# Kernel tuning notes

Measured on AMD Instinct MI355X. Metric: run time of the kernel, lower is better.

The kernel has to match this reference:

```python
import jax, jax.numpy as jnp
import numpy as np

N_EMBD = 1024
N_HEAD = 16
HEAD_DIM = N_EMBD // N_HEAD
D_FF = 4 * N_EMBD
B, T = 2, 2048


def setup_inputs() -> dict:
    key = jax.random.key(0)
    ks = jax.random.split(key, 16)
    s = 0.02
    d = {
        'x': jax.random.normal(ks[0], (B, T, N_EMBD), jnp.float32),
        'ln1_g': jnp.ones((N_EMBD,), jnp.float32),
        'ln1_b': jnp.zeros((N_EMBD,), jnp.float32),
        'Wq': jax.random.normal(ks[1], (N_EMBD, N_EMBD), jnp.float32) * s,
        'bq': jnp.zeros((N_EMBD,), jnp.float32),
        'Wk': jax.random.normal(ks[2], (N_EMBD, N_EMBD), jnp.float32) * s,
        'bk': jnp.zeros((N_EMBD,), jnp.float32),
        'Wv': jax.random.normal(ks[3], (N_EMBD, N_EMBD), jnp.float32) * s,
        'bv': jnp.zeros((N_EMBD,), jnp.float32),
        'Wo': jax.random.normal(ks[4], (N_EMBD, N_EMBD), jnp.float32) * s,
        'bo': jnp.zeros((N_EMBD,), jnp.float32),
        'ln2_g': jnp.ones((N_EMBD,), jnp.float32),
        'ln2_b': jnp.zeros((N_EMBD,), jnp.float32),
        'W1': jax.random.normal(ks[5], (N_EMBD, D_FF), jnp.float32) * s,
        'b1': jnp.zeros((D_FF,), jnp.float32),
        'W2': jax.random.normal(ks[6], (D_FF, N_EMBD), jnp.float32) * s,
        'b2': jnp.zeros((N_EMBD,), jnp.float32),
    }
    return d


def _layernorm(x, g, b, eps=1e-5):
    mu = jnp.mean(x, axis=-1, keepdims=True)
    var = jnp.var(x, axis=-1, keepdims=True)
    return (x - mu) * jax.lax.rsqrt(var + eps) * g + b


def _attention(x, Wq, bq, Wk, bk, Wv, bv, Wo, bo):
    b, t, c = x.shape
    q = (x @ Wq + bq).reshape(b, t, N_HEAD, HEAD_DIM).transpose(0, 2, 1, 3)
    k = (x @ Wk + bk).reshape(b, t, N_HEAD, HEAD_DIM).transpose(0, 2, 1, 3)
    v = (x @ Wv + bv).reshape(b, t, N_HEAD, HEAD_DIM).transpose(0, 2, 1, 3)
    att = jnp.einsum('bhqd,bhkd->bhqk', q, k) / jnp.sqrt(jnp.float32(HEAD_DIM))
    causal = jnp.tril(jnp.ones((t, t), bool))
    att = jnp.where(causal[None, None], att, -jnp.inf)
    att = jax.nn.softmax(att, axis=-1)
    y = jnp.einsum('bhqk,bhkd->bhqd', att, v)
    y = y.transpose(0, 2, 1, 3).reshape(b, t, c)
    return y @ Wo + bo


def reference(x, ln1_g, ln1_b, Wq, bq, Wk, bk, Wv, bv, Wo, bo, ln2_g, ln2_b, W1, b1, W2, b2):
    x = x + _attention(_layernorm(x, ln1_g, ln1_b), Wq, bq, Wk, bk, Wv, bv, Wo, bo)
    h = _layernorm(x, ln2_g, ln2_b)
    h = jax.nn.gelu(h @ W1 + b1, approximate=False) @ W2 + b2
    return x + h
```

## Files before the change

### kernel.cpp

```cpp
#include <hip/hip_runtime.h>
#include <hip/hip_bf16.h>

typedef __hip_bfloat16 bf16;
using bf16x8 = __attribute__((ext_vector_type(8))) short;
using f32x4  = __attribute__((ext_vector_type(4))) float;
using f32x16 = __attribute__((ext_vector_type(16))) float;
using u32x4  = __attribute__((ext_vector_type(4))) unsigned int;

#define TSEQ 2048
#define NH   16
#define HD   64
#define NC   1024
#define DFF  4096
#define NROWS 4096

__device__ __forceinline__ void load_lds16(const bf16* g, bf16* l) {
  __builtin_amdgcn_global_load_lds(
      (const __attribute__((address_space(1))) unsigned int*)g,
      (__attribute__((address_space(3))) unsigned int*)l, 16, 0, 0);
}

__device__ __forceinline__ float b2f(short s) {
  unsigned int u = ((unsigned int)(unsigned short)s) << 16;
  return __builtin_bit_cast(float, u);
}

__device__ __forceinline__ unsigned cvtpk(float a, float b) {
  unsigned r;
  asm("v_cvt_pk_bf16_f32 %0, %1, %2" : "=v"(r) : "v"(a), "v"(b));
  return r;
}

__device__ __forceinline__ void pl32swap(unsigned &d, unsigned &s) {
  asm("v_permlane32_swap_b32 %0, %1" : "+v"(d), "+v"(s));
}

__device__ __forceinline__ float gelu_f(float x) {
  float u = 0.7978845608028654f * fmaf(0.044715f * x, x * x, x);
  float e = __expf(2.0f * u);
  float t = 1.0f - 2.0f / (e + 1.0f);
  return 0.5f * x * (1.0f + t);
}

__global__ __launch_bounds__(256)
void ln_cast_kernel(const float* __restrict__ x, const float* __restrict__ g,
                    const float* __restrict__ b, bf16* __restrict__ out) {
  int row = blockIdx.x, tid = threadIdx.x;
  const float4 v = ((const float4*)(x + (size_t)row * NC))[tid];
  float s  = v.x + v.y + v.z + v.w;
  float s2 = v.x*v.x + v.y*v.y + v.z*v.z + v.w*v.w;
#pragma unroll
  for (int m = 1; m < 64; m <<= 1) { s += __shfl_xor(s, m); s2 += __shfl_xor(s2, m); }
  __shared__ float rs[4], rs2[4];
  if ((tid & 63) == 0) { rs[tid >> 6] = s; rs2[tid >> 6] = s2; }
  __syncthreads();
  s  = rs[0] + rs[1] + rs[2] + rs[3];
  s2 = rs2[0] + rs2[1] + rs2[2] + rs2[3];
  float mu   = s * (1.0f / NC);
  float var  = s2 * (1.0f / NC) - mu * mu;
  float rstd = rsqrtf(var + 1e-5f);
  const float4 gv = ((const float4*)g)[tid];
  const float4 bv = ((const float4*)b)[tid];
  bf16* o = out + (size_t)row * NC + tid * 4;
  o[0] = __float2bfloat16((v.x - mu) * rstd * gv.x + bv.x);
  o[1] = __float2bfloat16((v.y - mu) * rstd * gv.y + bv.y);
  o[2] = __float2bfloat16((v.z - mu) * rstd * gv.z + bv.z);
  o[3] = __float2bfloat16((v.w - mu) * rstd * gv.w + bv.w);
}

__global__ __launch_bounds__(256)
void wo_ln_kernel(const float* __restrict__ x, const float* __restrict__ bo,
                  const bf16* __restrict__ P, const float* __restrict__ g,
                  const float* __restrict__ bln, float* __restrict__ x2,
                  bf16* __restrict__ xn2) {
  int row = blockIdx.x, tid = threadIdx.x;
  size_t base = (size_t)row * NC + tid * 4;
  const float4 xv = *(const float4*)(x + base);
  const float4 bv = ((const float4*)bo)[tid];
  short4 p0 = *(const short4*)((const short*)P + base);
  short4 p1 = *(const short4*)((const short*)P + (size_t)NROWS * NC + base);
  float v0 = xv.x + bv.x + b2f(p0.x) + b2f(p1.x);
  float v1 = xv.y + bv.y + b2f(p0.y) + b2f(p1.y);
  float v2 = xv.z + bv.z + b2f(p0.z) + b2f(p1.z);
  float v3 = xv.w + bv.w + b2f(p0.w) + b2f(p1.w);
  float4 ov = {v0, v1, v2, v3};
  *(float4*)(x2 + base) = ov;
  float s  = v0 + v1 + v2 + v3;
  float s2 = v0*v0 + v1*v1 + v2*v2 + v3*v3;
#pragma unroll
  for (int m = 1; m < 64; m <<= 1) { s += __shfl_xor(s, m); s2 += __shfl_xor(s2, m); }
  __shared__ float rs[4], rs2[4];
  if ((tid & 63) == 0) { rs[tid >> 6] = s; rs2[tid >> 6] = s2; }
  __syncthreads();
  s  = rs[0] + rs[1] + rs[2] + rs[3];
  s2 = rs2[0] + rs2[1] + rs2[2] + rs2[3];
  float mu   = s * (1.0f / NC);
  float var  = s2 * (1.0f / NC) - mu * mu;
  float rstd = rsqrtf(var + 1e-5f);
  const float4 gv = ((const float4*)g)[tid];
  const float4 lv = ((const float4*)bln)[tid];
  bf16* o = xn2 + base;
  o[0] = __float2bfloat16((v0 - mu) * rstd * gv.x + lv.x);
  o[1] = __float2bfloat16((v1 - mu) * rstd * gv.y + lv.y);
  o[2] = __float2bfloat16((v2 - mu) * rstd * gv.z + lv.z);
  o[3] = __float2bfloat16((v3 - mu) * rstd * gv.w + lv.w);
}

__global__ __launch_bounds__(256)
void w2_final_kernel(const float* __restrict__ x2, const float* __restrict__ b2,
                     const bf16* __restrict__ P, float* __restrict__ out) {
  int row = blockIdx.x, tid = threadIdx.x;
  size_t base = (size_t)row * NC + tid * 4;
  const float4 xv = *(const float4*)(x2 + base);
  const float4 bv = ((const float4*)b2)[tid];
  float a0 = xv.x + bv.x, a1 = xv.y + bv.y, a2 = xv.z + bv.z, a3 = xv.w + bv.w;
#pragma unroll
  for (int z = 0; z < 4; ++z) {
    short4 p = *(const short4*)((const short*)P + (size_t)z * NROWS * NC + base);
    a0 += b2f(p.x); a1 += b2f(p.y); a2 += b2f(p.z); a3 += b2f(p.w);
  }
  float4 ov = {a0, a1, a2, a3};
  *(float4*)(out + base) = ov;
}

__global__ __launch_bounds__(256)
void transpose_all_kernel(const float* __restrict__ Wq, const float* __restrict__ Wk,
                          const float* __restrict__ Wv, const float* __restrict__ Wo,
                          const float* __restrict__ W1, const float* __restrict__ W2,
                          bf16* __restrict__ WqkvoT, bf16* __restrict__ W1T,
                          bf16* __restrict__ W2T) {
  int bid = blockIdx.x;
  const float* W; bf16* Wt; int K, N, nx, tile;
  if (bid < 4096) {
    int z = bid >> 10; tile = bid & 1023;
    W = (z == 0) ? Wq : (z == 1) ? Wk : (z == 2) ? Wv : Wo;
    Wt = WqkvoT + (size_t)z * NC * NC; K = NC; N = NC; nx = 32;
  } else if (bid < 8192) {
    tile = bid - 4096; W = W1; Wt = W1T; K = NC; N = DFF; nx = 128;
  } else {
    tile = bid - 8192; W = W2; Wt = W2T; K = DFF; N = NC; nx = 32;
  }
  int n0 = (tile % nx) * 32, k0 = (tile / nx) * 32;
  __shared__ float t[32][33];
  int tx = threadIdx.x, ty = threadIdx.y;
#pragma unroll
  for (int i = 0; i < 4; ++i)
    t[ty + i * 8][tx] = W[(size_t)(k0 + ty + i * 8) * N + n0 + tx];
  __syncthreads();
#pragma unroll
  for (int i = 0; i < 4; ++i)
    Wt[(size_t)(n0 + ty + i * 8) * K + k0 + tx] = __float2bfloat16(t[tx][ty + i * 8]);
}

#define MODE_GELU 4
#define MODE_QKV  5
#define MODE_PART 6

template <int MODE>
__global__ __launch_bounds__(512, 2)
void gemm256(const bf16* __restrict__ A, const bf16* __restrict__ Bt,
             const float* __restrict__ bias, const float* __restrict__ bias2,
             const float* __restrict__ bias3,
             void* __restrict__ outp, void* __restrict__ out2, void* __restrict__ out3,
             int M, int N, int K, int KS) {
  __shared__ bf16 lds[65536];
  int tid  = threadIdx.x;
  int w    = tid >> 6;
  int lane = tid & 63;
  int l31  = lane & 31;
  int kb   = lane >> 5;
  int wm   = w >> 2, wn = w & 3;

  int gN = gridDim.x, gM = gridDim.y;
  int pid = blockIdx.y * gN + blockIdx.x;
  int npg = 4 * gN;
  int gid = pid / npg;
  int fm  = gid * 4;
  int gsz = min(gM - fm, 4);
  int bm = (fm + (pid % gsz)) * 256;
  int bn = ((pid % npg) / gsz) * 256;
  int k_beg = blockIdx.z * KS;

  int srow  = w * 32 + l31;
  int skoff = kb * 8;
  const bf16* sA[2]; const bf16* sB[2];
#pragma unroll
  for (int j = 0; j < 2; ++j) {
    sA[j] = A  + (size_t)(bm + srow) * K + k_beg + j * 16 + skoff;
    sB[j] = Bt + (size_t)(bn + srow) * K + k_beg + j * 16 + skoff;
  }

  auto stage = [&](int t) {
    int b = t & 3;
    bf16* dA = &lds[b * 8192];
    bf16* dB = &lds[32768 + b * 8192];
    int koff = t * 32;
#pragma unroll
    for (int j = 0; j < 2; ++j) {
      load_lds16(sA[j] + koff, dA + (w * 2 + j) * 512);
      load_lds16(sB[j] + koff, dB + (w * 2 + j) * 512);
    }
  };

  f32x16 acc[4][2];
#pragma unroll
  for (int mi = 0; mi < 4; ++mi)
#pragma unroll
    for (int ni = 0; ni < 2; ++ni)
#pragma unroll
      for (int r = 0; r < 16; ++r) acc[mi][ni][r] = 0.f;

  int NT = KS >> 5;
  stage(0); stage(1); stage(2);

  for (int t = 0; t < NT; ++t) {
    if (t < NT - 2)       asm volatile("s_waitcnt vmcnt(8)" ::: "memory");
    else if (t == NT - 2) asm volatile("s_waitcnt vmcnt(4)" ::: "memory");
    else                  asm volatile("s_waitcnt vmcnt(0)" ::: "memory");
    __builtin_amdgcn_s_barrier();
    asm volatile("" ::: "memory");
    if (t + 3 < NT) stage(t + 3);

    const bf16* bufA = &lds[(t & 3) * 8192];
    const bf16* bufB = &lds[32768 + (t & 3) * 8192];
    bf16x8 af[2][4], bfr[2][2];
#pragma unroll
    for (int ks = 0; ks < 2; ++ks) {
#pragma unroll
      for (int mi = 0; mi < 4; ++mi)
        af[ks][mi] = *(const bf16x8*)&bufA[((wm * 4 + mi) * 2 + ks) * 512 + lane * 8];
#pragma unroll
      for (int ni = 0; ni < 2; ++ni)
        bfr[ks][ni] = *(const bf16x8*)&bufB[((wn * 2 + ni) * 2 + ks) * 512 + lane * 8];
    }
    __builtin_amdgcn_s_setprio(1);
#pragma unroll
    for (int ks = 0; ks < 2; ++ks)
#pragma unroll
      for (int mi = 0; mi < 4; ++mi)
#pragma unroll
        for (int ni = 0; ni < 2; ++ni)
          acc[mi][ni] = __builtin_amdgcn_mfma_f32_32x32x16_bf16(af[ks][mi], bfr[ks][ni], acc[mi][ni], 0, 0, 0);
    __builtin_amdgcn_s_setprio(0);
  }

  if (MODE == MODE_PART) {
    bf16* dst = (bf16*)outp + (size_t)blockIdx.z * M * N;
#pragma unroll
    for (int mi = 0; mi < 4; ++mi)
#pragma unroll
      for (int ni = 0; ni < 2; ++ni) {
        int col = bn + wn * 64 + ni * 32 + l31;
#pragma unroll
        for (int reg = 0; reg < 16; ++reg) {
          int row = bm + wm * 128 + mi * 32 + (reg & 3) + 8 * (reg >> 2) + 4 * kb;
          dst[(size_t)row * N + col] = __float2bfloat16(acc[mi][ni][reg]);
        }
      }
  } else if (MODE == MODE_GELU) {
    float bcol[2];
#pragma unroll
    for (int ni = 0; ni < 2; ++ni) bcol[ni] = bias[bn + wn * 64 + ni * 32 + l31];
#pragma unroll
    for (int mi = 0; mi < 4; ++mi)
#pragma unroll
      for (int ni = 0; ni < 2; ++ni) {
        int col = bn + wn * 64 + ni * 32 + l31;
#pragma unroll
        for (int reg = 0; reg < 16; ++reg) {
          int row = bm + wm * 128 + mi * 32 + (reg & 3) + 8 * (reg >> 2) + 4 * kb;
          ((bf16*)outp)[(size_t)row * N + col] =
              __float2bfloat16(gelu_f(acc[mi][ni][reg] + bcol[ni]));
        }
      }
  } else {
    int seg = bn >> 10;
    int c1b = (bn & (NC - 1)) + wn * 64;
    const float* bp = (seg == 0) ? bias : (seg == 1) ? bias2 : bias3;
    float bcol[2]; int hh[2], dd[2];
#pragma unroll
    for (int ni = 0; ni < 2; ++ni) {
      int c1 = c1b + ni * 32 + l31;
      bcol[ni] = bp[c1]; hh[ni] = c1 >> 6; dd[ni] = c1 & (HD - 1);
    }
    if (seg == 0) {
      bf16* dst = (bf16*)outp;
#pragma unroll
      for (int mi = 0; mi < 4; ++mi)
#pragma unroll
        for (int reg = 0; reg < 16; ++reg) {
          int row = bm + wm * 128 + mi * 32 + (reg & 3) + 8 * (reg >> 2) + 4 * kb;
          int bbi = row >> 11, t = row & (TSEQ - 1);
#pragma unroll
          for (int ni = 0; ni < 2; ++ni)
            dst[((size_t)(bbi * NH + hh[ni]) * TSEQ + t) * HD + dd[ni]] =
                __float2bfloat16(acc[mi][ni][reg] + bcol[ni]);
        }
    } else if (seg == 1) {
      bf16* dst = (bf16*)out2;
#pragma unroll
      for (int mi = 0; mi < 4; ++mi)
#pragma unroll
        for (int reg = 0; reg < 16; ++reg) {
          int row = bm + wm * 128 + mi * 32 + (reg & 3) + 8 * (reg >> 2) + 4 * kb;
          int bbi = row >> 11, t = row & (TSEQ - 1);
          int kt = t >> 5, lk = t & 31;
#pragma unroll
          for (int ni = 0; ni < 2; ++ni) {
            int d = dd[ni];
            size_t off = ((((size_t)(bbi * NH + hh[ni]) * 64 + kt) * 4 + (d >> 4)) * 64
                          + ((d >> 3) & 1) * 32 + lk) * 8 + (d & 7);
            dst[off] = __float2bfloat16(acc[mi][ni][reg] + bcol[ni]);
          }
        }
    } else {
      bf16* dst = (bf16*)out3;
#pragma unroll
      for (int mi = 0; mi < 4; ++mi)
#pragma unroll
        for (int reg = 0; reg < 16; ++reg) {
          int row = bm + wm * 128 + mi * 32 + (reg & 3) + 8 * (reg >> 2) + 4 * kb;
          int bbi = row >> 11, t = row & (TSEQ - 1);
          int kt = t >> 5, rem = t & 31;
          int ks = rem >> 4, hf = (rem >> 3) & 1, j = rem & 7;
#pragma unroll
          for (int ni = 0; ni < 2; ++ni) {
            int d = dd[ni];
            size_t off = (((((size_t)(bbi * NH + hh[ni]) * 64 + kt) * 2 + (d >> 5)) * 2 + ks) * 64
                          + hf * 32 + (d & 31)) * 8 + j;
            dst[off] = __float2bfloat16(acc[mi][ni][reg] + bcol[ni]);
          }
        }
    }
  }
}

__global__ __launch_bounds__(256)
void attn_kernel(const bf16* __restrict__ q, const bf16* __restrict__ kf,
                 const bf16* __restrict__ vf, bf16* __restrict__ out) {
  int id  = blockIdx.x;
  int xcd = id & 7;
  int t   = id >> 3;
  int bh  = xcd * 4 + (t & 3);
  int u   = t >> 2;
  int qt  = (u < 32) ? (2 * u) : (63 - 2 * (u - 32));
  int b = bh >> 4, h = bh & 15;

  int tid  = threadIdx.x;
  int w    = tid >> 6;
  int lane = tid & 63;
  int l31  = lane & 31;
  int hh   = lane >> 5;
  int h8   = hh * 8;
  int base4 = hh * 4;

  const bf16* qp  = q  + (size_t)(b * NH + h) * TSEQ * HD;
  const bf16* kfb = kf + (size_t)bh * (64 * 4 * 64 * 8);
  const bf16* vfb = vf + (size_t)bh * (64 * 2 * 2 * 64 * 8);

  int q0 = qt * 32;

  bf16x8 qf[4];
#pragma unroll
  for (int ds = 0; ds < 4; ++ds)
    qf[ds] = *(const bf16x8*)(qp + (size_t)(q0 + l31) * HD + ds * 16 + h8);

  f32x16 o0, o1;
#pragma unroll
  for (int r = 0; r < 16; ++r) { o0[r] = 0.f; o1[r] = 0.f; }
  float lacc = 0.f;

  bf16x8 a0, a1, a2, a3;

  auto step = [&](int kt, bool dg) {
    const bf16* vs = vfb + (size_t)kt * 2048 + lane * 8;
    bf16x8 v00 = *(const bf16x8*)(vs);
    bf16x8 v01 = *(const bf16x8*)(vs + 512);
    bf16x8 v10 = *(const bf16x8*)(vs + 1024);
    bf16x8 v11 = *(const bf16x8*)(vs + 1536);
    bf16x8 n0, n1, n2, n3;
    bool pf = !dg && (kt + 4 <= qt);
    if (pf) {
      const bf16* kn = kfb + (size_t)(kt + 4) * 2048 + lane * 8;
      n0 = *(const bf16x8*)(kn);
      n1 = *(const bf16x8*)(kn + 512);
      n2 = *(const bf16x8*)(kn + 1024);
      n3 = *(const bf16x8*)(kn + 1536);
    }

    f32x16 c;
#pragma unroll
    for (int r = 0; r < 16; ++r) c[r] = 0.f;
    c = __builtin_amdgcn_mfma_f32_32x32x16_bf16(a0, qf[0], c, 0, 0, 0);
    c = __builtin_amdgcn_mfma_f32_32x32x16_bf16(a1, qf[1], c, 0, 0, 0);
    c = __builtin_amdgcn_mfma_f32_32x32x16_bf16(a2, qf[2], c, 0, 0, 0);
    c = __builtin_amdgcn_mfma_f32_32x32x16_bf16(a3, qf[3], c, 0, 0, 0);

    float p[16];
    float ls = 0.f;
#pragma unroll
    for (int r = 0; r < 16; ++r) {
      float pv = exp2f(fmaf(c[r], 0.18033688011112042f, -11.541560327111707f));
      if (dg) {
        int krr = (r & 3) + 8 * (r >> 2) + base4;
        pv = (krr <= l31) ? pv : 0.f;
      }
      p[r] = pv;
      ls += pv;
    }
    lacc += ls;

    unsigned A0 = cvtpk(p[0],  p[1]),  C0 = cvtpk(p[4],  p[5]);
    unsigned B0 = cvtpk(p[2],  p[3]),  D0 = cvtpk(p[6],  p[7]);
    pl32swap(A0, C0); pl32swap(B0, D0);
    unsigned A1 = cvtpk(p[8],  p[9]),  C1 = cvtpk(p[12], p[13]);
    unsigned B1 = cvtpk(p[10], p[11]), D1 = cvtpk(p[14], p[15]);
    pl32swap(A1, C1); pl32swap(B1, D1);
    u32x4 w0v = {A0, B0, C0, D0};
    u32x4 w1v = {A1, B1, C1, D1};
    bf16x8 pa0 = __builtin_bit_cast(bf16x8, w0v);
    bf16x8 pa1 = __builtin_bit_cast(bf16x8, w1v);

    o0 = __builtin_amdgcn_mfma_f32_32x32x16_bf16(pa0, v00, o0, 0, 0, 0);
    o0 = __builtin_amdgcn_mfma_f32_32x32x16_bf16(pa1, v01, o0, 0, 0, 0);
    o1 = __builtin_amdgcn_mfma_f32_32x32x16_bf16(pa0, v10, o1, 0, 0, 0);
    o1 = __builtin_amdgcn_mfma_f32_32x32x16_bf16(pa1, v11, o1, 0, 0, 0);

    if (pf) { a0 = n0; a1 = n1; a2 = n2; a3 = n3; }
  };

  if (w <= qt) {
    const bf16* ka = kfb + (size_t)w * 2048 + lane * 8;
    a0 = *(const bf16x8*)(ka);
    a1 = *(const bf16x8*)(ka + 512);
    a2 = *(const bf16x8*)(ka + 1024);
    a3 = *(const bf16x8*)(ka + 1536);
    int diag = (w == (qt & 3)) ? 1 : 0;
    int T = ((qt - w) >> 2) + 1 - diag;
    int kt = w;
    for (int i = 0; i < T; ++i, kt += 4) step(kt, false);
    if (diag) step(qt, true);
  }

  __shared__ float red[2][64][33];
  auto dump = [&](int slot) {
    float* d = &red[slot][lane][0];
#pragma unroll
    for (int r = 0; r < 16; ++r) { d[r] = o0[r]; d[16 + r] = o1[r]; }
    d[32] = lacc;
  };
  auto gather = [&](int slot) {
    const float* s = &red[slot][lane][0];
#pragma unroll
    for (int r = 0; r < 16; ++r) { o0[r] += s[r]; o1[r] += s[16 + r]; }
    lacc += s[32];
  };
  if (w >= 2) dump(w - 2);
  __syncthreads();
  if (w < 2) gather(w);
  __syncthreads();
  if (w == 1) dump(0);
  __syncthreads();
  if (w == 0) {
    gather(0);
    float ltot = lacc + __shfl_xor(lacc, 32);
    float linv = 1.0f / ltot;
#pragma unroll
    for (int r = 0; r < 16; ++r) {
      int qoff = (r & 3) + 8 * (r >> 2) + base4;
      float sc = __shfl(linv, qoff);
      size_t ob = ((size_t)(b * TSEQ + q0 + qoff)) * NC + h * HD + l31;
      out[ob]      = __float2bfloat16(o0[r] * sc);
      out[ob + 32] = __float2bfloat16(o1[r] * sc);
    }
  }
}

extern "C" void kernel_launch(void* const* d_in, const int* in_sizes, int n_in,
                              void* d_out, int out_size, void* d_ws, size_t ws_size,
                              hipStream_t stream) {
  const float* x     = (const float*)d_in[0];
  const float* ln1_g = (const float*)d_in[1];
  const float* ln1_b = (const float*)d_in[2];
  const float* Wq    = (const float*)d_in[3];
  const float* bq    = (const float*)d_in[4];
  const float* Wk    = (const float*)d_in[5];
  const float* bk    = (const float*)d_in[6];
  const float* Wv    = (const float*)d_in[7];
  const float* bv    = (const float*)d_in[8];
  const float* Wo    = (const float*)d_in[9];
  const float* bo    = (const float*)d_in[10];
  const float* ln2_g = (const float*)d_in[11];
  const float* ln2_b = (const float*)d_in[12];
  const float* W1    = (const float*)d_in[13];
  const float* b1    = (const float*)d_in[14];
  const float* W2    = (const float*)d_in[15];
  const float* b2    = (const float*)d_in[16];

  char* ws = (char*)d_ws;
  const size_t MB = 1u << 20;
  bf16* WqkvT = (bf16*)(ws + 0 * MB);
  bf16* W1T  = (bf16*)(ws + 8 * MB);
  bf16* W2T  = (bf16*)(ws + 16 * MB);
  bf16* xn1  = (bf16*)(ws + 24 * MB);
  bf16* qb   = (bf16*)(ws + 32 * MB);
  bf16* kfB  = (bf16*)(ws + 40 * MB);
  bf16* vfB  = (bf16*)(ws + 48 * MB);
  bf16* att  = (bf16*)(ws + 56 * MB);
  float* x2  = (float*)(ws + 64 * MB);
  bf16* xn2  = (bf16*)(ws + 80 * MB);
  bf16* h1   = (bf16*)(ws + 88 * MB);
  bf16* woP  = (bf16*)(ws + 88 * MB);
  bf16* w2P  = (bf16*)(ws + 32 * MB);
  bf16* WoT  = WqkvT + 3 * (size_t)NC * NC;

  transpose_all_kernel<<<12288, dim3(32, 8), 0, stream>>>(
      Wq, Wk, Wv, Wo, W1, W2, WqkvT, W1T, W2T);

  ln_cast_kernel<<<NROWS, 256, 0, stream>>>(x, ln1_g, ln1_b, xn1);

  gemm256<MODE_QKV><<<dim3(12, 16, 1), 512, 0, stream>>>(
      xn1, WqkvT, bq, bk, bv, qb, kfB, vfB, NROWS, 3 * NC, NC, NC);

  attn_kernel<<<2048, 256, 0, stream>>>(qb, kfB, vfB, att);

  gemm256<MODE_PART><<<dim3(4, 16, 2), 512, 0, stream>>>(
      att, WoT, nullptr, nullptr, nullptr, woP, nullptr, nullptr, NROWS, NC, NC, NC / 2);

  wo_ln_kernel<<<NROWS, 256, 0, stream>>>(x, bo, woP, ln2_g, ln2_b, x2, xn2);

  gemm256<MODE_GELU><<<dim3(16, 16, 1), 512, 0, stream>>>(
      xn2, W1T, b1, nullptr, nullptr, h1, nullptr, nullptr, NROWS, DFF, NC, NC);

  gemm256<MODE_PART><<<dim3(4, 16, 4), 512, 0, stream>>>(
      h1, W2T, nullptr, nullptr, nullptr, w2P, nullptr, nullptr, NROWS, NC, DFF, DFF / 4);

  w2_final_kernel<<<NROWS, 256, 0, stream>>>(x2, b2, w2P, (float*)d_out);
}
```

Before: 357.1 us.

## Split GEMM main loop into two half-K phases with interleaved A/B staging

Result: faster. 346.4 us (-3.0%).

```diff
diff --git a/kernel.cpp b/kernel.cpp
--- a/kernel.cpp
+++ b/kernel.cpp
@@ -190,17 +190,18 @@
     sB[j] = Bt + (size_t)(bn + srow) * K + k_beg + j * 16 + skoff;
   }
 
-  auto stage = [&](int t) {
-    int b = t & 3;
-    bf16* dA = &lds[b * 8192];
-    bf16* dB = &lds[32768 + b * 8192];
+  auto stageA = [&](int t) {
+    bf16* dA = &lds[(t & 3) * 8192];
     int koff = t * 32;
-#pragma unroll
-    for (int j = 0; j < 2; ++j) {
-      load_lds16(sA[j] + koff, dA + (w * 2 + j) * 512);
-      load_lds16(sB[j] + koff, dB + (w * 2 + j) * 512);
-    }
+    load_lds16(sA[0] + koff, dA + (w * 2 + 0) * 512);
+    load_lds16(sA[1] + koff, dA + (w * 2 + 1) * 512);
   };
+  auto stageB = [&](int t) {
+    bf16* dB = &lds[32768 + (t & 3) * 8192];
+    int koff = t * 32;
+    load_lds16(sB[0] + koff, dB + (w * 2 + 0) * 512);
+    load_lds16(sB[1] + koff, dB + (w * 2 + 1) * 512);
+  };
 
   f32x16 acc[4][2];
 #pragma unroll
@@ -211,36 +212,54 @@
       for (int r = 0; r < 16; ++r) acc[mi][ni][r] = 0.f;
 
   int NT = KS >> 5;
-  stage(0); stage(1); stage(2);
+  stageA(0); stageB(0); stageA(1); stageB(1); stageA(2); stageB(2);
 
   for (int t = 0; t < NT; ++t) {
     if (t < NT - 2)       asm volatile("s_waitcnt vmcnt(8)" ::: "memory");
     else if (t == NT - 2) asm volatile("s_waitcnt vmcnt(4)" ::: "memory");
     else                  asm volatile("s_waitcnt vmcnt(0)" ::: "memory");
     __builtin_amdgcn_s_barrier();
-    asm volatile("" ::: "memory");
-    if (t + 3 < NT) stage(t + 3);
 
     const bf16* bufA = &lds[(t & 3) * 8192];
     const bf16* bufB = &lds[32768 + (t & 3) * 8192];
-    bf16x8 af[2][4], bfr[2][2];
-#pragma unroll
-    for (int ks = 0; ks < 2; ++ks) {
-#pragma unroll
-      for (int mi = 0; mi < 4; ++mi)
-        af[ks][mi] = *(const bf16x8*)&bufA[((wm * 4 + mi) * 2 + ks) * 512 + lane * 8];
+
+    bf16x8 af0[4], bf0[2];
+#pragma unroll
+    for (int mi = 0; mi < 4; ++mi)
+      af0[mi] = *(const bf16x8*)&bufA[((wm * 4 + mi) * 2 + 0) * 512 + lane * 8];
+#pragma unroll
+    for (int ni = 0; ni < 2; ++ni)
+      bf0[ni] = *(const bf16x8*)&bufB[((wn * 2 + ni) * 2 + 0) * 512 + lane * 8];
+    if (t + 3 < NT) stageA(t + 3);
+    __builtin_amdgcn_s_barrier();
+    asm volatile("s_waitcnt lgkmcnt(0)" ::: "memory");
+    __builtin_amdgcn_sched_barrier(0);
+    __builtin_amdgcn_s_setprio(1);
+#pragma unroll
+    for (int mi = 0; mi < 4; ++mi)
 #pragma unroll
       for (int ni = 0; ni < 2; ++ni)
-        bfr[ks][ni] = *(const bf16x8*)&bufB[((wn * 2 + ni) * 2 + ks) * 512 + lane * 8];
-    }
+        acc[mi][ni] = __builtin_amdgcn_mfma_f32_32x32x16_bf16(af0[mi], bf0[ni], acc[mi][ni], 0, 0, 0);
+    __builtin_amdgcn_s_setprio(0);
+    __builtin_amdgcn_s_barrier();
+
+    bf16x8 af1[4], bf1[2];
+#pragma unroll
+    for (int mi = 0; mi < 4; ++mi)
+      af1[mi] = *(const bf16x8*)&bufA[((wm * 4 + mi) * 2 + 1) * 512 + lane * 8];
+#pragma unroll
+    for (int ni = 0; ni < 2; ++ni)
+      bf1[ni] = *(const bf16x8*)&bufB[((wn * 2 + ni) * 2 + 1) * 512 + lane * 8];
+    if (t + 3 < NT) stageB(t + 3);
+    __builtin_amdgcn_s_barrier();
+    asm volatile("s_waitcnt lgkmcnt(0)" ::: "memory");
+    __builtin_amdgcn_sched_barrier(0);
     __builtin_amdgcn_s_setprio(1);
 #pragma unroll
-    for (int ks = 0; ks < 2; ++ks)
-#pragma unroll
-      for (int mi = 0; mi < 4; ++mi)
-#pragma unroll
-        for (int ni = 0; ni < 2; ++ni)
-          acc[mi][ni] = __builtin_amdgcn_mfma_f32_32x32x16_bf16(af[ks][mi], bfr[ks][ni], acc[mi][ni], 0, 0, 0);
+    for (int mi = 0; mi < 4; ++mi)
+#pragma unroll
+      for (int ni = 0; ni < 2; ++ni)
+        acc[mi][ni] = __builtin_amdgcn_mfma_f32_32x32x16_bf16(af1[mi], bf1[ni], acc[mi][ni], 0, 0, 0);
     __builtin_amdgcn_s_setprio(0);
   }
 
```

## Replace direct global-to-LDS 4-stage pipeline with register-staged double buffering

Applied to the files above, without the earlier changes.

New measurement: 339.1 us. 5.0% less time.

```diff
diff --git a/kernel.cpp b/kernel.cpp
--- a/kernel.cpp
+++ b/kernel.cpp
@@ -13,12 +13,6 @@
 #define NC   1024
 #define DFF  4096
 #define NROWS 4096
-
-__device__ __forceinline__ void load_lds16(const bf16* g, bf16* l) {
-  __builtin_amdgcn_global_load_lds(
-      (const __attribute__((address_space(1))) unsigned int*)g,
-      (__attribute__((address_space(3))) unsigned int*)l, 16, 0, 0);
-}
 
 __device__ __forceinline__ float b2f(short s) {
   unsigned int u = ((unsigned int)(unsigned short)s) << 16;
@@ -163,7 +157,7 @@
              const float* __restrict__ bias3,
              void* __restrict__ outp, void* __restrict__ out2, void* __restrict__ out3,
              int M, int N, int K, int KS) {
-  __shared__ bf16 lds[65536];
+  __shared__ bf16 lds[32768];
   int tid  = threadIdx.x;
   int w    = tid >> 6;
   int lane = tid & 63;
@@ -181,26 +175,17 @@
   int bn = ((pid % npg) / gsz) * 256;
   int k_beg = blockIdx.z * KS;
 
-  int srow  = w * 32 + l31;
-  int skoff = kb * 8;
-  const bf16* sA[2]; const bf16* sB[2];
-#pragma unroll
-  for (int j = 0; j < 2; ++j) {
-    sA[j] = A  + (size_t)(bm + srow) * K + k_beg + j * 16 + skoff;
-    sB[j] = Bt + (size_t)(bn + srow) * K + k_beg + j * 16 + skoff;
-  }
-
-  auto stage = [&](int t) {
-    int b = t & 3;
-    bf16* dA = &lds[b * 8192];
-    bf16* dB = &lds[32768 + b * 8192];
-    int koff = t * 32;
-#pragma unroll
-    for (int j = 0; j < 2; ++j) {
-      load_lds16(sA[j] + koff, dA + (w * 2 + j) * 512);
-      load_lds16(sB[j] + koff, dB + (w * 2 + j) * 512);
-    }
-  };
+  int c = lane & 3;
+  int q = lane >> 2;
+  const bf16* gA = A  + (size_t)(bm + w * 32 + q) * K + k_beg + c * 8;
+  const bf16* gB = Bt + (size_t)(bn + w * 32 + q) * K + k_beg + c * 8;
+  int wr = (w * 2 + (c >> 1)) * 512 + ((c & 1) * 32 + q) * 8;
+
+  bf16x8 ra0, ra1, rb0, rb1;
+  ra0 = *(const bf16x8*)(gA);
+  ra1 = *(const bf16x8*)(gA + (size_t)16 * K);
+  rb0 = *(const bf16x8*)(gB);
+  rb1 = *(const bf16x8*)(gB + (size_t)16 * K);
 
   f32x16 acc[4][2];
 #pragma unroll
@@ -211,18 +196,27 @@
       for (int r = 0; r < 16; ++r) acc[mi][ni][r] = 0.f;
 
   int NT = KS >> 5;
-  stage(0); stage(1); stage(2);
-
   for (int t = 0; t < NT; ++t) {
-    if (t < NT - 2)       asm volatile("s_waitcnt vmcnt(8)" ::: "memory");
-    else if (t == NT - 2) asm volatile("s_waitcnt vmcnt(4)" ::: "memory");
-    else                  asm volatile("s_waitcnt vmcnt(0)" ::: "memory");
+    bf16* dA = &lds[(t & 1) * 8192];
+    bf16* dB = &lds[16384 + (t & 1) * 8192];
+    *(bf16x8*)(dA + wr)       = ra0;
+    *(bf16x8*)(dA + wr + 128) = ra1;
+    *(bf16x8*)(dB + wr)       = rb0;
+    *(bf16x8*)(dB + wr + 128) = rb1;
+    if (t + 1 < NT) {
+      size_t ko = (size_t)(t + 1) * 32;
+      ra0 = *(const bf16x8*)(gA + ko);
+      ra1 = *(const bf16x8*)(gA + ko + (size_t)16 * K);
+      rb0 = *(const bf16x8*)(gB + ko);
+      rb1 = *(const bf16x8*)(gB + ko + (size_t)16 * K);
+    }
+    __builtin_amdgcn_sched_barrier(0);
+    asm volatile("s_waitcnt lgkmcnt(0)" ::: "memory");
     __builtin_amdgcn_s_barrier();
-    asm volatile("" ::: "memory");
-    if (t + 3 < NT) stage(t + 3);
-
-    const bf16* bufA = &lds[(t & 3) * 8192];
-    const bf16* bufB = &lds[32768 + (t & 3) * 8192];
+    __builtin_amdgcn_sched_barrier(0);
+
+    const bf16* bufA = &lds[(t & 1) * 8192];
+    const bf16* bufB = &lds[16384 + (t & 1) * 8192];
     bf16x8 af[2][4], bfr[2][2];
 #pragma unroll
     for (int ks = 0; ks < 2; ++ks) {
```
